# Kernel tuning notes

Hardware: AMD Instinct MI355X
Metric: run time of the kernel (lower is better)

The kernel has to match this reference:

```python
import jax, jax.numpy as jnp
import numpy as np

B, LA, LB = 16, 2048, 2048
DA, DB, DH = 768, 512, 512
EPS = 1e-5


def _layer_norm(x, g, b):
    mu = jnp.mean(x, axis=-1, keepdims=True)
    var = jnp.var(x, axis=-1, keepdims=True)
    return (x - mu) * jax.lax.rsqrt(var + EPS) * g + b


def setup_inputs() -> dict:
    key = jax.random.key(0)
    ks = jax.random.split(key, 12)
    s = lambda d: 1.0 / np.sqrt(d)
    return {
        "z_a": jax.random.normal(ks[0], (B, LA, DA), jnp.float32),
        "z_b": jax.random.normal(ks[1], (B, LB, DB), jnp.float32),
        "Wa": jax.random.uniform(ks[2], (DA, DH), jnp.float32, -s(DA), s(DA)),
        "ba": jnp.zeros((DH,), jnp.float32),
        "Wb": jax.random.uniform(ks[3], (DB, DH), jnp.float32, -s(DB), s(DB)),
        "bb": jnp.zeros((DH,), jnp.float32),
        "W_co": jax.random.normal(ks[4], (DH, DH), jnp.float32),
        "Woa": jax.random.uniform(ks[5], (DH, DA), jnp.float32, -s(DH), s(DH)),
        "boa": jnp.zeros((DA,), jnp.float32),
        "Wob": jax.random.uniform(ks[6], (DH, DB), jnp.float32, -s(DH), s(DH)),
        "bob": jnp.zeros((DB,), jnp.float32),
        "ga": jnp.ones((DA,), jnp.float32),
        "beta_a": jnp.zeros((DA,), jnp.float32),
        "gb": jnp.ones((DB,), jnp.float32),
        "beta_b": jnp.zeros((DB,), jnp.float32),
    }


def reference(z_a, z_b, Wa, ba, Wb, bb, W_co, Woa, boa, Wob, bob, ga, beta_a, gb, beta_b):
    # projections to shared hidden space
    h_a = jnp.einsum('bld,dh->blh', z_a, Wa) + ba          # (B, LA, DH)
    h_b = jnp.einsum('bld,dh->blh', z_b, Wb) + bb          # (B, LB, DH)
    # bilinear tanh co-attention scores
    C = jnp.tanh(jnp.einsum('bih,hk,bjk->bij', h_a, W_co, h_b))  # (B, LA, LB)
    attn_a = jax.nn.softmax(C, axis=-1)                    # rows: over LB
    attn_b = jax.nn.softmax(C.transpose(0, 2, 1), axis=-1) # cols: over LA
    h_a_co = jnp.einsum('bij,bjh->bih', attn_a, h_b)       # (B, LA, DH)
    h_b_co = jnp.einsum('bji,bih->bjh', attn_b, h_a)       # (B, LB, DH)
    z_a_co = jnp.einsum('blh,hd->bld', h_a_co, Woa) + boa
    z_b_co = jnp.einsum('blh,hd->bld', h_b_co, Wob) + bob
    z_a_out = _layer_norm(z_a + z_a_co, ga, beta_a)
    z_b_out = _layer_norm(z_b + z_b_co, gb, beta_b)
    return (z_a_out, z_b_out)
```

## Files before the change

kernel.cpp:

```cpp
#include <hip/hip_runtime.h>
#include <stdint.h>

typedef short bf16x8 __attribute__((ext_vector_type(8)));
typedef float f32x4 __attribute__((ext_vector_type(4)));

#define BM 128
#define BN 128
#define BK 64

#define AS1 __attribute__((address_space(1)))
#define AS3 __attribute__((address_space(3)))

__device__ __forceinline__ ushort f2bf(float x) {
    uint32_t u = __float_as_uint(x);
    u += 0x7FFFu + ((u >> 16) & 1u);
    return (ushort)(u >> 16);
}

__device__ __forceinline__ void gload16(const void* g, void* l) {
    __builtin_amdgcn_global_load_lds((const AS1 void*)g, (AS3 void*)l, 16, 0, 0);
}

template<int MODE, bool HAS_BIAS, bool WRITE_T>
__global__ __launch_bounds__(256)
void gemm_bt(const ushort* __restrict__ Aptr_, const ushort* __restrict__ Bptr_,
             void* __restrict__ Cptr_, ushort* __restrict__ CTptr_,
             const float* __restrict__ bias, const float* __restrict__ resid_,
             float* __restrict__ rsum_, float* __restrict__ csum_,
             const float* __restrict__ scale_,
             int M, int N, int K, int lda, int ldb, int ldc,
             long sA, long sB, long sC, long sCT, long sSum,
             int ldct, int rbshift)
{
    __shared__ ushort Alds[2][BM * BK];
    __shared__ ushort Blds[2][BN * BK];

    const int z    = blockIdx.z;
    const int m0   = blockIdx.x * BM;
    const int n0   = blockIdx.y * BN;
    const int tid  = threadIdx.x;
    const int lane = tid & 63;
    const int wave = tid >> 6;
    const int wr   = wave >> 1, wc = wave & 1;
    const int g    = lane >> 4, c = lane & 15;

    const ushort* Ap = Aptr_ + z * sA;
    const ushort* Bp = Bptr_ + z * sB;

    f32x4 acc[4][4] = {};

    auto stage = [&](int ktoff, int buf) {
        #pragma unroll
        for (int r = 0; r < 4; ++r) {
            const int li  = r * 256 + tid;
            const int row = li >> 3;
            const int gck = (li & 7) ^ (row & 7);
            gload16(Ap + (long)(m0 + row) * lda + ktoff + gck * 8, &Alds[buf][li * 8]);
            gload16(Bp + (long)(n0 + row) * ldb + ktoff + gck * 8, &Blds[buf][li * 8]);
        }
    };

    const int nk = K / BK;
    stage(0, 0);
    int cur = 0;
    for (int t = 0; t < nk; ++t) {
        if (t + 1 < nk) {
            stage((t + 1) * BK, cur ^ 1);
            asm volatile("s_waitcnt vmcnt(8)" ::: "memory");
        } else {
            asm volatile("s_waitcnt vmcnt(0)" ::: "memory");
        }
        __builtin_amdgcn_s_barrier();

        #pragma unroll
        for (int kk = 0; kk < 2; ++kk) {
            bf16x8 af[4], bfr[4];
            #pragma unroll
            for (int mi = 0; mi < 4; ++mi) {
                const int row = wr * 64 + mi * 16 + c;
                const int ckq = (kk * 4 + g) ^ (row & 7);
                af[mi] = *(const bf16x8*)&Alds[cur][row * BK + ckq * 8];
            }
            #pragma unroll
            for (int ni = 0; ni < 4; ++ni) {
                const int row = wc * 64 + ni * 16 + c;
                const int ckq = (kk * 4 + g) ^ (row & 7);
                bfr[ni] = *(const bf16x8*)&Blds[cur][row * BK + ckq * 8];
            }
            #pragma unroll
            for (int mi = 0; mi < 4; ++mi)
                #pragma unroll
                for (int ni = 0; ni < 4; ++ni)
                    acc[mi][ni] = __builtin_amdgcn_mfma_f32_16x16x32_bf16(af[mi], bfr[ni], acc[mi][ni], 0, 0, 0);
        }

        asm volatile("s_waitcnt lgkmcnt(0)" ::: "memory");
        __builtin_amdgcn_s_barrier();
        cur ^= 1;
    }

    if constexpr (MODE == 0) {
        ushort* Cp = (ushort*)Cptr_ + z * sC;
        #pragma unroll
        for (int mi = 0; mi < 4; ++mi) {
            const int row = m0 + wr * 64 + mi * 16 + g * 4;
            #pragma unroll
            for (int ni = 0; ni < 4; ++ni) {
                const int col = n0 + wc * 64 + ni * 16 + c;
                const float bv = HAS_BIAS ? bias[col] : 0.f;
                ushort v[4];
                #pragma unroll
                for (int r = 0; r < 4; ++r) v[r] = f2bf(acc[mi][ni][r] + bv);
                #pragma unroll
                for (int r = 0; r < 4; ++r) Cp[(long)(row + r) * ldc + col] = v[r];
                if constexpr (WRITE_T) {
                    const int bb = row >> rbshift;
                    const int ii = row & ((1 << rbshift) - 1);
                    *(ushort4*)&CTptr_[(long)bb * sCT + (long)col * ldct + ii] =
                        make_ushort4(v[0], v[1], v[2], v[3]);
                }
            }
        }
    } else if constexpr (MODE == 1) {
        ushort* Ep  = (ushort*)Cptr_ + z * sC;
        ushort* ETp = CTptr_ + z * sCT;
        float* rs = rsum_ + z * sSum;
        float* cs = csum_ + z * sSum;
        float rowpart[4][4] = {};
        float colpart[4] = {};
        #pragma unroll
        for (int mi = 0; mi < 4; ++mi) {
            const int row = m0 + wr * 64 + mi * 16 + g * 4;
            #pragma unroll
            for (int ni = 0; ni < 4; ++ni) {
                const int col = n0 + wc * 64 + ni * 16 + c;
                ushort v[4];
                #pragma unroll
                for (int r = 0; r < 4; ++r) {
                    const float s = acc[mi][ni][r];
                    const float t = 1.f - 2.f / (__expf(2.f * s) + 1.f);
                    const float e = __expf(t);
                    rowpart[mi][r] += e;
                    colpart[ni]    += e;
                    v[r] = f2bf(e);
                }
                #pragma unroll
                for (int r = 0; r < 4; ++r) Ep[(long)(row + r) * ldc + col] = v[r];
                *(ushort4*)&ETp[(long)col * ldct + row] = make_ushort4(v[0], v[1], v[2], v[3]);
            }
        }
        #pragma unroll
        for (int mi = 0; mi < 4; ++mi) {
            #pragma unroll
            for (int r = 0; r < 4; ++r) {
                float v = rowpart[mi][r];
                v += __shfl_xor(v, 1); v += __shfl_xor(v, 2);
                v += __shfl_xor(v, 4); v += __shfl_xor(v, 8);
                if (c == 0) atomicAdd(&rs[m0 + wr * 64 + mi * 16 + g * 4 + r], v);
            }
        }
        #pragma unroll
        for (int ni = 0; ni < 4; ++ni) {
            float v = colpart[ni];
            v += __shfl_xor(v, 16); v += __shfl_xor(v, 32);
            if (g == 0) atomicAdd(&cs[n0 + wc * 64 + ni * 16 + c], v);
        }
    } else if constexpr (MODE == 2) {
        const float* sc = scale_ + z * sSum;
        ushort* Cp = (ushort*)Cptr_ + z * sC;
        #pragma unroll
        for (int mi = 0; mi < 4; ++mi) {
            const int row = m0 + wr * 64 + mi * 16 + g * 4;
            float rcp[4];
            #pragma unroll
            for (int r = 0; r < 4; ++r) rcp[r] = 1.f / sc[row + r];
            #pragma unroll
            for (int ni = 0; ni < 4; ++ni) {
                const int col = n0 + wc * 64 + ni * 16 + c;
                #pragma unroll
                for (int r = 0; r < 4; ++r)
                    Cp[(long)(row + r) * ldc + col] = f2bf(acc[mi][ni][r] * rcp[r]);
            }
        }
    } else {
        float* Co = (float*)Cptr_;
        #pragma unroll
        for (int mi = 0; mi < 4; ++mi) {
            const int row = m0 + wr * 64 + mi * 16 + g * 4;
            #pragma unroll
            for (int ni = 0; ni < 4; ++ni) {
                const int col = n0 + wc * 64 + ni * 16 + c;
                const float bv = bias[col];
                #pragma unroll
                for (int r = 0; r < 4; ++r) {
                    const long idx = (long)(row + r) * ldc + col;
                    Co[idx] = acc[mi][ni][r] + bv + resid_[idx];
                }
            }
        }
    }
}

__global__ __launch_bounds__(256)
void cast32to16(const float* __restrict__ in, ushort* __restrict__ out, long n) {
    const long stride = (long)gridDim.x * 256 * 8;
    for (long i = ((long)blockIdx.x * 256 + threadIdx.x) * 8; i < n; i += stride) {
        const float4 f0 = *(const float4*)(in + i);
        const float4 f1 = *(const float4*)(in + i + 4);
        uint4 w;
        w.x = (uint)f2bf(f0.x) | ((uint)f2bf(f0.y) << 16);
        w.y = (uint)f2bf(f0.z) | ((uint)f2bf(f0.w) << 16);
        w.z = (uint)f2bf(f1.x) | ((uint)f2bf(f1.y) << 16);
        w.w = (uint)f2bf(f1.z) | ((uint)f2bf(f1.w) << 16);
        *(uint4*)(out + i) = w;
    }
}

__global__ __launch_bounds__(256)
void tcast(const float* __restrict__ in, ushort* __restrict__ out, int R, int C) {
    __shared__ float t[32][33];
    const int bx = blockIdx.x * 32, by = blockIdx.y * 32;
    const int tx = threadIdx.x, ty = threadIdx.y;
    for (int i = ty; i < 32; i += 8) {
        const int r = by + i, cc = bx + tx;
        if (r < R && cc < C) t[i][tx] = in[(long)r * C + cc];
    }
    __syncthreads();
    for (int i = ty; i < 32; i += 8) {
        const int cc = bx + i, r = by + tx;
        if (cc < C && r < R) out[(long)cc * R + r] = f2bf(t[tx][i]);
    }
}

template<int D>
__global__ __launch_bounds__(256)
void ln_rows(float* __restrict__ y, const float* __restrict__ gam, const float* __restrict__ bet) {
    constexpr int NV = D / 256;
    const long row = blockIdx.x;
    float* p = y + row * D;
    const int tid = threadIdx.x;
    float v[NV];
    float s = 0.f, s2 = 0.f;
    #pragma unroll
    for (int k = 0; k < NV; ++k) {
        v[k] = p[tid + k * 256];
        s += v[k]; s2 += v[k] * v[k];
    }
    #pragma unroll
    for (int off = 1; off < 64; off <<= 1) {
        s  += __shfl_xor(s, off);
        s2 += __shfl_xor(s2, off);
    }
    __shared__ float ws[4], ws2[4];
    const int wave = tid >> 6, lane = tid & 63;
    if (lane == 0) { ws[wave] = s; ws2[wave] = s2; }
    __syncthreads();
    s  = ws[0] + ws[1] + ws[2] + ws[3];
    s2 = ws2[0] + ws2[1] + ws2[2] + ws2[3];
    const float mu  = s / D;
    const float var = s2 / D - mu * mu;
    const float rstd = rsqrtf(var + 1e-5f);
    #pragma unroll
    for (int k = 0; k < NV; ++k) {
        const int i = tid + k * 256;
        p[i] = (v[k] - mu) * rstd * gam[i] + bet[i];
    }
}

extern "C" void kernel_launch(void* const* d_in, const int* in_sizes, int n_in,
                              void* d_out, int out_size, void* d_ws, size_t ws_size,
                              hipStream_t stream)
{
    (void)in_sizes; (void)n_in; (void)out_size; (void)ws_size;
    const float* z_a    = (const float*)d_in[0];
    const float* z_b    = (const float*)d_in[1];
    const float* Wa     = (const float*)d_in[2];
    const float* ba     = (const float*)d_in[3];
    const float* Wb     = (const float*)d_in[4];
    const float* bb     = (const float*)d_in[5];
    const float* Wco    = (const float*)d_in[6];
    const float* Woa    = (const float*)d_in[7];
    const float* boa    = (const float*)d_in[8];
    const float* Wob    = (const float*)d_in[9];
    const float* bob    = (const float*)d_in[10];
    const float* ga     = (const float*)d_in[11];
    const float* beta_a = (const float*)d_in[12];
    const float* gb     = (const float*)d_in[13];
    const float* beta_b = (const float*)d_in[14];

    const int Bn = 16, LA = 2048, LB = 2048, DA = 768, DB = 512, DH = 512;
    const long MA = (long)Bn * LA;
    const long MB = (long)Bn * LB;

    char* w = (char*)d_ws;
    size_t off = 0;
    auto alc = [&](size_t bytes) { void* p = w + off; off += (bytes + 255) & ~(size_t)255; return p; };

    ushort* WaT  = (ushort*)alc((size_t)DH * DA * 2);
    ushort* WbT  = (ushort*)alc((size_t)DH * DB * 2);
    ushort* WcoT = (ushort*)alc((size_t)DH * DH * 2);
    ushort* WoaT = (ushort*)alc((size_t)DA * DH * 2);
    ushort* WobT = (ushort*)alc((size_t)DB * DH * 2);
    ushort* h_a  = (ushort*)alc((size_t)MA * DH * 2);
    ushort* h_b  = (ushort*)alc((size_t)MB * DH * 2);
    ushort* h_aT = (ushort*)alc((size_t)Bn * DH * LA * 2);
    ushort* h_bT = (ushort*)alc((size_t)Bn * DH * LB * 2);
    ushort* Ma   = (ushort*)alc((size_t)MA * DH * 2);
    ushort* E    = (ushort*)alc((size_t)Bn * LA * LB * 2);
    ushort* ET   = (ushort*)alc((size_t)Bn * LB * LA * 2);
    ushort* Pa   = (ushort*)alc((size_t)MA * DH * 2);
    ushort* Pb   = (ushort*)alc((size_t)MB * DH * 2);
    float*  rsum = (float*)alc((size_t)Bn * LA * 4);
    float*  csum = (float*)alc((size_t)Bn * LB * 4);

    ushort* za16 = E;
    ushort* zb16 = E + (size_t)MA * DA;

    dim3 blk(256, 1, 1);
    dim3 tb(32, 8, 1);

    tcast<<<dim3(DH / 32, DA / 32, 1), tb, 0, stream>>>(Wa,  WaT,  DA, DH);
    tcast<<<dim3(DH / 32, DB / 32, 1), tb, 0, stream>>>(Wb,  WbT,  DB, DH);
    tcast<<<dim3(DH / 32, DH / 32, 1), tb, 0, stream>>>(Wco, WcoT, DH, DH);
    tcast<<<dim3(DA / 32, DH / 32, 1), tb, 0, stream>>>(Woa, WoaT, DH, DA);
    tcast<<<dim3(DB / 32, DH / 32, 1), tb, 0, stream>>>(Wob, WobT, DH, DB);

    cast32to16<<<dim3(2048, 1, 1), blk, 0, stream>>>(z_a, za16, MA * DA);
    cast32to16<<<dim3(2048, 1, 1), blk, 0, stream>>>(z_b, zb16, MB * DB);

    hipMemsetAsync(rsum, 0, (size_t)Bn * (LA + LB) * sizeof(float), stream);

    gemm_bt<0, true, true><<<dim3(MA / BM, DH / BN, 1), blk, 0, stream>>>(
        za16, WaT, h_a, h_aT, ba, nullptr, nullptr, nullptr, nullptr,
        (int)MA, DH, DA, DA, DA, DH, 0, 0, 0, (long)DH * LA, 0, LA, 11);

    gemm_bt<0, true, true><<<dim3(MB / BM, DH / BN, 1), blk, 0, stream>>>(
        zb16, WbT, h_b, h_bT, bb, nullptr, nullptr, nullptr, nullptr,
        (int)MB, DH, DB, DB, DB, DH, 0, 0, 0, (long)DH * LB, 0, LB, 11);

    gemm_bt<0, false, false><<<dim3(MA / BM, DH / BN, 1), blk, 0, stream>>>(
        h_a, WcoT, Ma, nullptr, nullptr, nullptr, nullptr, nullptr, nullptr,
        (int)MA, DH, DH, DH, DH, DH, 0, 0, 0, 0, 0, 0, 0);

    gemm_bt<1, false, false><<<dim3(LA / BM, LB / BN, Bn), blk, 0, stream>>>(
        Ma, h_b, E, ET, nullptr, nullptr, rsum, csum, nullptr,
        LA, LB, DH, DH, DH, LB,
        (long)LA * DH, (long)LB * DH, (long)LA * LB, (long)LB * LA, LA, LA, 0);

    gemm_bt<2, false, false><<<dim3(LA / BM, DH / BN, Bn), blk, 0, stream>>>(
        E, h_bT, Pa, nullptr, nullptr, nullptr, nullptr, nullptr, rsum,
        LA, DH, LB, LB, LB, DH,
        (long)LA * LB, (long)DH * LB, (long)LA * DH, 0, LA, 0, 0);

    gemm_bt<2, false, false><<<dim3(LB / BM, DH / BN, Bn), blk, 0, stream>>>(
        ET, h_aT, Pb, nullptr, nullptr, nullptr, nullptr, nullptr, csum,
        LB, DH, LA, LA, LA, DH,
        (long)LB * LA, (long)DH * LA, (long)LB * DH, 0, LB, 0, 0);

    float* outA = (float*)d_out;
    float* outB = outA + MA * DA;

    gemm_bt<3, true, false><<<dim3(MA / BM, DA / BN, 1), blk, 0, stream>>>(
        Pa, WoaT, outA, nullptr, boa, z_a, nullptr, nullptr, nullptr,
        (int)MA, DA, DH, DH, DH, DA, 0, 0, 0, 0, 0, 0, 0);

    gemm_bt<3, true, false><<<dim3(MB / BM, DB / BN, 1), blk, 0, stream>>>(
        Pb, WobT, outB, nullptr, bob, z_b, nullptr, nullptr, nullptr,
        (int)MB, DB, DH, DH, DH, DB, 0, 0, 0, 0, 0, 0, 0);

    ln_rows<768><<<dim3((unsigned)MA, 1, 1), blk, 0, stream>>>(outA, ga, beta_a);
    ln_rows<512><<<dim3((unsigned)MB, 1, 1), blk, 0, stream>>>(outB, gb, beta_b);
}
```

Before: 811.9 us.

## Enlarge GEMM tile to 256x128 with 8 waves and triple-buffered LDS pipeline

```diff
diff --git a/kernel.cpp b/kernel.cpp
--- a/kernel.cpp
+++ b/kernel.cpp
@@ -4,9 +4,11 @@
 typedef short bf16x8 __attribute__((ext_vector_type(8)));
 typedef float f32x4 __attribute__((ext_vector_type(4)));
 
-#define BM 128
+#define BM 256
 #define BN 128
 #define BK 64
+#define ABUF_U 16384
+#define BUF_U  24576
 
 #define AS1 __attribute__((address_space(1)))
 #define AS3 __attribute__((address_space(3)))
@@ -22,7 +24,7 @@
 }
 
 template<int MODE, bool HAS_BIAS, bool WRITE_T>
-__global__ __launch_bounds__(256)
+__global__ __launch_bounds__(512)
 void gemm_bt(const ushort* __restrict__ Aptr_, const ushort* __restrict__ Bptr_,
              void* __restrict__ Cptr_, ushort* __restrict__ CTptr_,
              const float* __restrict__ bias, const float* __restrict__ resid_,
@@ -32,8 +34,7 @@
              long sA, long sB, long sC, long sCT, long sSum,
              int ldct, int rbshift)
 {
-    __shared__ ushort Alds[2][BM * BK];
-    __shared__ ushort Blds[2][BN * BK];
+    extern __shared__ ushort smem[];
 
     const int z    = blockIdx.z;
     const int m0   = blockIdx.x * BM;
@@ -41,72 +42,106 @@
     const int tid  = threadIdx.x;
     const int lane = tid & 63;
     const int wave = tid >> 6;
-    const int wr   = wave >> 1, wc = wave & 1;
+    const int wr   = wave >> 2;
+    const int wcn  = wave & 3;
     const int g    = lane >> 4, c = lane & 15;
 
     const ushort* Ap = Aptr_ + z * sA;
     const ushort* Bp = Bptr_ + z * sB;
 
-    f32x4 acc[4][4] = {};
-
-    auto stage = [&](int ktoff, int buf) {
-        #pragma unroll
-        for (int r = 0; r < 4; ++r) {
-            const int li  = r * 256 + tid;
-            const int row = li >> 3;
-            const int gck = (li & 7) ^ (row & 7);
-            gload16(Ap + (long)(m0 + row) * lda + ktoff + gck * 8, &Alds[buf][li * 8]);
-            gload16(Bp + (long)(n0 + row) * ldb + ktoff + gck * 8, &Blds[buf][li * 8]);
+    long aoff[4]; int aLds[4];
+    #pragma unroll
+    for (int u = 0; u < 4; ++u) {
+        const int li  = u * 512 + tid;
+        const int row = li >> 3;
+        const int gck = (li & 7) ^ (row & 7);
+        aoff[u] = (long)(m0 + row) * lda + gck * 8;
+        aLds[u] = li * 8;
+    }
+    long boff[2]; int bLds[2];
+    #pragma unroll
+    for (int v = 0; v < 2; ++v) {
+        const int li  = v * 512 + tid;
+        const int row = li >> 3;
+        const int gck = (li & 7) ^ (row & 7);
+        boff[v] = (long)(n0 + row) * ldb + gck * 8;
+        bLds[v] = li * 8;
+    }
+
+    auto stage3 = [&](int kt, ushort* As, ushort* Bs, int q) {
+        if (q == 0) {
+            gload16(Ap + aoff[0] + kt, As + aLds[0]);
+            gload16(Ap + aoff[1] + kt, As + aLds[1]);
+            gload16(Ap + aoff[2] + kt, As + aLds[2]);
+        } else {
+            gload16(Ap + aoff[3] + kt, As + aLds[3]);
+            gload16(Bp + boff[0] + kt, Bs + bLds[0]);
+            gload16(Bp + boff[1] + kt, Bs + bLds[1]);
         }
     };
 
+    f32x4 acc[8][2] = {};
+
     const int nk = K / BK;
-    stage(0, 0);
-    int cur = 0;
+    stage3(0, smem, smem + ABUF_U, 0);
+    stage3(0, smem, smem + ABUF_U, 1);
+    stage3(BK, smem + BUF_U, smem + BUF_U + ABUF_U, 0);
+    stage3(BK, smem + BUF_U, smem + BUF_U + ABUF_U, 1);
+    asm volatile("s_waitcnt vmcnt(6)" ::: "memory");
+    __builtin_amdgcn_s_barrier();
+
+    int bt = 0;
     for (int t = 0; t < nk; ++t) {
-        if (t + 1 < nk) {
-            stage((t + 1) * BK, cur ^ 1);
-            asm volatile("s_waitcnt vmcnt(8)" ::: "memory");
-        } else {
-            asm volatile("s_waitcnt vmcnt(0)" ::: "memory");
-        }
-        __builtin_amdgcn_s_barrier();
-
-        #pragma unroll
-        for (int kk = 0; kk < 2; ++kk) {
-            bf16x8 af[4], bfr[4];
-            #pragma unroll
-            for (int mi = 0; mi < 4; ++mi) {
-                const int row = wr * 64 + mi * 16 + c;
-                const int ckq = (kk * 4 + g) ^ (row & 7);
-                af[mi] = *(const bf16x8*)&Alds[cur][row * BK + ckq * 8];
-            }
-            #pragma unroll
-            for (int ni = 0; ni < 4; ++ni) {
-                const int row = wc * 64 + ni * 16 + c;
-                const int ckq = (kk * 4 + g) ^ (row & 7);
-                bfr[ni] = *(const bf16x8*)&Blds[cur][row * BK + ckq * 8];
-            }
-            #pragma unroll
-            for (int mi = 0; mi < 4; ++mi)
-                #pragma unroll
-                for (int ni = 0; ni < 4; ++ni)
+        const int b2 = (bt + 2 >= 3) ? bt - 1 : bt + 2;
+        ushort* As  = smem + bt * BUF_U;
+        ushort* Bs  = As + ABUF_U;
+        ushort* As2 = smem + b2 * BUF_U;
+        ushort* Bs2 = As2 + ABUF_U;
+        const bool pf = (t + 2 < nk);
+
+        #pragma unroll
+        for (int q = 0; q < 2; ++q) {
+            bf16x8 af[8], bfr[2];
+            #pragma unroll
+            for (int mi = 0; mi < 8; ++mi) {
+                const int row = wr * 128 + mi * 16 + c;
+                const int ckq = (q * 4 + g) ^ (row & 7);
+                af[mi] = *(const bf16x8*)&As[row * BK + ckq * 8];
+            }
+            #pragma unroll
+            for (int ni = 0; ni < 2; ++ni) {
+                const int row = wcn * 32 + ni * 16 + c;
+                const int ckq = (q * 4 + g) ^ (row & 7);
+                bfr[ni] = *(const bf16x8*)&Bs[row * BK + ckq * 8];
+            }
+            if (pf) stage3((t + 2) * BK, As2, Bs2, q);
+            if (q == 1) {
+                if (pf) asm volatile("s_waitcnt vmcnt(6)" ::: "memory");
+                else    asm volatile("s_waitcnt vmcnt(0)" ::: "memory");
+            }
+            asm volatile("" ::: "memory");
+            __builtin_amdgcn_s_barrier();
+            __builtin_amdgcn_s_setprio(1);
+            #pragma unroll
+            for (int mi = 0; mi < 8; ++mi)
+                #pragma unroll
+                for (int ni = 0; ni < 2; ++ni)
                     acc[mi][ni] = __builtin_amdgcn_mfma_f32_16x16x32_bf16(af[mi], bfr[ni], acc[mi][ni], 0, 0, 0);
-        }
-
-        asm volatile("s_waitcnt lgkmcnt(0)" ::: "memory");
-        __builtin_amdgcn_s_barrier();
-        cur ^= 1;
+            __builtin_amdgcn_s_setprio(0);
+            asm volatile("" ::: "memory");
+            __builtin_amdgcn_s_barrier();
+        }
+        bt = (bt + 1 == 3) ? 0 : bt + 1;
     }
 
     if constexpr (MODE == 0) {
         ushort* Cp = (ushort*)Cptr_ + z * sC;
         #pragma unroll
-        for (int mi = 0; mi < 4; ++mi) {
-            const int row = m0 + wr * 64 + mi * 16 + g * 4;
-            #pragma unroll
-            for (int ni = 0; ni < 4; ++ni) {
-                const int col = n0 + wc * 64 + ni * 16 + c;
+        for (int mi = 0; mi < 8; ++mi) {
+            const int row = m0 + wr * 128 + mi * 16 + g * 4;
+            #pragma unroll
+            for (int ni = 0; ni < 2; ++ni) {
+                const int col = n0 + wcn * 32 + ni * 16 + c;
                 const float bv = HAS_BIAS ? bias[col] : 0.f;
                 ushort v[4];
                 #pragma unroll
@@ -126,14 +161,14 @@
         ushort* ETp = CTptr_ + z * sCT;
         float* rs = rsum_ + z * sSum;
         float* cs = csum_ + z * sSum;
-        float rowpart[4][4] = {};
-        float colpart[4] = {};
-        #pragma unroll
-        for (int mi = 0; mi < 4; ++mi) {
-            const int row = m0 + wr * 64 + mi * 16 + g * 4;
-            #pragma unroll
-            for (int ni = 0; ni < 4; ++ni) {
-                const int col = n0 + wc * 64 + ni * 16 + c;
+        float rowpart[8][4] = {};
+        float colpart[2] = {};
+        #pragma unroll
+        for (int mi = 0; mi < 8; ++mi) {
+            const int row = m0 + wr * 128 + mi * 16 + g * 4;
+            #pragma unroll
+            for (int ni = 0; ni < 2; ++ni) {
+                const int col = n0 + wcn * 32 + ni * 16 + c;
                 ushort v[4];
                 #pragma unroll
                 for (int r = 0; r < 4; ++r) {
@@ -150,33 +185,33 @@
             }
         }
         #pragma unroll
-        for (int mi = 0; mi < 4; ++mi) {
+        for (int mi = 0; mi < 8; ++mi) {
             #pragma unroll
             for (int r = 0; r < 4; ++r) {
                 float v = rowpart[mi][r];
                 v += __shfl_xor(v, 1); v += __shfl_xor(v, 2);
                 v += __shfl_xor(v, 4); v += __shfl_xor(v, 8);
-                if (c == 0) atomicAdd(&rs[m0 + wr * 64 + mi * 16 + g * 4 + r], v);
-            }
-        }
-        #pragma unroll
-        for (int ni = 0; ni < 4; ++ni) {
+                if (c == 0) atomicAdd(&rs[m0 + wr * 128 + mi * 16 + g * 4 + r], v);
+            }
+        }
+        #pragma unroll
+        for (int ni = 0; ni < 2; ++ni) {
             float v = colpart[ni];
             v += __shfl_xor(v, 16); v += __shfl_xor(v, 32);
-            if (g == 0) atomicAdd(&cs[n0 + wc * 64 + ni * 16 + c], v);
+            if (g == 0) atomicAdd(&cs[n0 + wcn * 32 + ni * 16 + c], v);
         }
     } else if constexpr (MODE == 2) {
         const float* sc = scale_ + z * sSum;
         ushort* Cp = (ushort*)Cptr_ + z * sC;
         #pragma unroll
-        for (int mi = 0; mi < 4; ++mi) {
-            const int row = m0 + wr * 64 + mi * 16 + g * 4;
+        for (int mi = 0; mi < 8; ++mi) {
+            const int row = m0 + wr * 128 + mi * 16 + g * 4;
             float rcp[4];
             #pragma unroll
             for (int r = 0; r < 4; ++r) rcp[r] = 1.f / sc[row + r];
             #pragma unroll
-            for (int ni = 0; ni < 4; ++ni) {
-                const int col = n0 + wc * 64 + ni * 16 + c;
+            for (int ni = 0; ni < 2; ++ni) {
+                const int col = n0 + wcn * 32 + ni * 16 + c;
                 #pragma unroll
                 for (int r = 0; r < 4; ++r)
                     Cp[(long)(row + r) * ldc + col] = f2bf(acc[mi][ni][r] * rcp[r]);
@@ -185,11 +220,11 @@
     } else {
         float* Co = (float*)Cptr_;
         #pragma unroll
-        for (int mi = 0; mi < 4; ++mi) {
-            const int row = m0 + wr * 64 + mi * 16 + g * 4;
-            #pragma unroll
-            for (int ni = 0; ni < 4; ++ni) {
-                const int col = n0 + wc * 64 + ni * 16 + c;
+        for (int mi = 0; mi < 8; ++mi) {
+            const int row = m0 + wr * 128 + mi * 16 + g * 4;
+            #pragma unroll
+            for (int ni = 0; ni < 2; ++ni) {
+                const int col = n0 + wcn * 32 + ni * 16 + c;
                 const float bv = bias[col];
                 #pragma unroll
                 for (int r = 0; r < 4; ++r) {
@@ -316,8 +351,10 @@
     ushort* za16 = E;
     ushort* zb16 = E + (size_t)MA * DA;
 
-    dim3 blk(256, 1, 1);
+    dim3 blk(512, 1, 1);
+    dim3 blk256(256, 1, 1);
     dim3 tb(32, 8, 1);
+    const int SHM = 3 * BUF_U * 2;
 
     tcast<<<dim3(DH / 32, DA / 32, 1), tb, 0, stream>>>(Wa,  WaT,  DA, DH);
     tcast<<<dim3(DH / 32, DB / 32, 1), tb, 0, stream>>>(Wb,  WbT,  DB, DH);
@@ -325,34 +362,34 @@
     tcast<<<dim3(DA / 32, DH / 32, 1), tb, 0, stream>>>(Woa, WoaT, DH, DA);
     tcast<<<dim3(DB / 32, DH / 32, 1), tb, 0, stream>>>(Wob, WobT, DH, DB);
 
-    cast32to16<<<dim3(2048, 1, 1), blk, 0, stream>>>(z_a, za16, MA * DA);
-    cast32to16<<<dim3(2048, 1, 1), blk, 0, stream>>>(z_b, zb16, MB * DB);
+    cast32to16<<<dim3(2048, 1, 1), blk256, 0, stream>>>(z_a, za16, MA * DA);
+    cast32to16<<<dim3(2048, 1, 1), blk256, 0, stream>>>(z_b, zb16, MB * DB);
 
     hipMemsetAsync(rsum, 0, (size_t)Bn * (LA + LB) * sizeof(float), stream);
 
-    gemm_bt<0, true, true><<<dim3(MA / BM, DH / BN, 1), blk, 0, stream>>>(
+    gemm_bt<0, true, true><<<dim3(MA / BM, DH / BN, 1), blk, SHM, stream>>>(
         za16, WaT, h_a, h_aT, ba, nullptr, nullptr, nullptr, nullptr,
         (int)MA, DH, DA, DA, DA, DH, 0, 0, 0, (long)DH * LA, 0, LA, 11);
 
-    gemm_bt<0, true, true><<<dim3(MB / BM, DH / BN, 1), blk, 0, stream>>>(
+    gemm_bt<0, true, true><<<dim3(MB / BM, DH / BN, 1), blk, SHM, stream>>>(
         zb16, WbT, h_b, h_bT, bb, nullptr, nullptr, nullptr, nullptr,
         (int)MB, DH, DB, DB, DB, DH, 0, 0, 0, (long)DH * LB, 0, LB, 11);
 
-    gemm_bt<0, false, false><<<dim3(MA / BM, DH / BN, 1), blk, 0, stream>>>(
+    gemm_bt<0, false, false><<<dim3(MA / BM, DH / BN, 1), blk, SHM, stream>>>(
         h_a, WcoT, Ma, nullptr, nullptr, nullptr, nullptr, nullptr, nullptr,
         (int)MA, DH, DH, DH, DH, DH, 0, 0, 0, 0, 0, 0, 0);
 
-    gemm_bt<1, false, false><<<dim3(LA / BM, LB / BN, Bn), blk, 0, stream>>>(
+    gemm_bt<1, false, false><<<dim3(LA / BM, LB / BN, Bn), blk, SHM, stream>>>(
         Ma, h_b, E, ET, nullptr, nullptr, rsum, csum, nullptr,
         LA, LB, DH, DH, DH, LB,
         (long)LA * DH, (long)LB * DH, (long)LA * LB, (long)LB * LA, LA, LA, 0);
 
-    gemm_bt<2, false, false><<<dim3(LA / BM, DH / BN, Bn), blk, 0, stream>>>(
+    gemm_bt<2, false, false><<<dim3(LA / BM, DH / BN, Bn), blk, SHM, stream>>>(
         E, h_bT, Pa, nullptr, nullptr, nullptr, nullptr, nullptr, rsum,
         LA, DH, LB, LB, LB, DH,
         (long)LA * LB, (long)DH * LB, (long)LA * DH, 0, LA, 0, 0);
 
-    gemm_bt<2, false, false><<<dim3(LB / BM, DH / BN, Bn), blk, 0, stream>>>(
+    gemm_bt<2, false, false><<<dim3(LB / BM, DH / BN, Bn), blk, SHM, stream>>>(
         ET, h_aT, Pb, nullptr, nullptr, nullptr, nullptr, nullptr, csum,
         LB, DH, LA, LA, LA, DH,
         (long)LB * LA, (long)DH * LA, (long)LB * DH, 0, LB, 0, 0);
@@ -360,14 +397,14 @@
     float* outA = (float*)d_out;
     float* outB = outA + MA * DA;
 
-    gemm_bt<3, true, false><<<dim3(MA / BM, DA / BN, 1), blk, 0, stream>>>(
+    gemm_bt<3, true, false><<<dim3(MA / BM, DA / BN, 1), blk, SHM, stream>>>(
         Pa, WoaT, outA, nullptr, boa, z_a, nullptr, nullptr, nullptr,
         (int)MA, DA, DH, DH, DH, DA, 0, 0, 0, 0, 0, 0, 0);
 
-    gemm_bt<3, true, false><<<dim3(MB / BM, DB / BN, 1), blk, 0, stream>>>(
+    gemm_bt<3, true, false><<<dim3(MB / BM, DB / BN, 1), blk, SHM, stream>>>(
         Pb, WobT, outB, nullptr, bob, z_b, nullptr, nullptr, nullptr,
         (int)MB, DB, DH, DH, DH, DB, 0, 0, 0, 0, 0, 0, 0);
 
-    ln_rows<768><<<dim3((unsigned)MA, 1, 1), blk, 0, stream>>>(outA, ga, beta_a);
-    ln_rows<512><<<dim3((unsigned)MB, 1, 1), blk, 0, stream>>>(outB, gb, beta_b);
-}
+    ln_rows<768><<<dim3((unsigned)MA, 1, 1), blk256, 0, stream>>>(outA, ga, beta_a);
+    ln_rows<512><<<dim3((unsigned)MB, 1, 1), blk256, 0, stream>>>(outB, gb, beta_b);
+}
```

Result: faster. 781.6 us (-3.7%).
